# Performance work log

Measured on AMD Instinct MI355X. Metric: run time of the kernel, lower is better.

The kernel has to match this reference:

```python
import jax, jax.numpy as jnp
import numpy as np

K = 3  # kernel_size

def _extract_patches(x):
    # x: (b, n, h, w) -> (b, n, K*K, h, w), stride=1, padding=1 (zeros), row-major kernel order like nn.Unfold
    b, n, h, w = x.shape
    xp = jnp.pad(x, ((0, 0), (0, 0), (1, 1), (1, 1)))
    slices = [xp[:, :, i:i + h, j:j + w] for i in range(K) for j in range(K)]
    return jnp.stack(slices, axis=2)

def _conv3x3(x, w, b):
    # x: (b, cin, h, w), w: (cout, cin, 3, 3)
    y = jax.lax.conv_general_dilated(
        x, w, window_strides=(1, 1), padding=((1, 1), (1, 1)),
        dimension_numbers=('NCHW', 'OIHW', 'NCHW'))
    return y + b[None, :, None, None]

def setup_inputs() -> dict:
    key = jax.random.key(0)
    ks = jax.random.split(key, 6)
    b, n, h, w = 8, 256, 64, 64
    cout, r = 256, 4
    cm = n // r
    s = lambda fan: 1.0 / np.sqrt(fan)
    return {
        'x':    jax.random.normal(ks[0], (b, n, h, w), jnp.float32),
        'w_c1': jax.random.normal(ks[1], (cm, n), jnp.float32) * s(n),
        'b_c1': jnp.zeros((cm,), jnp.float32),
        'w_c2': jax.random.normal(ks[2], (n, cm), jnp.float32) * s(cm),
        'b_c2': jnp.zeros((n,), jnp.float32),
        'w_d1': jax.random.normal(ks[3], (cm, n, 3, 3), jnp.float32) * s(n * 9),
        'b_d1': jnp.zeros((cm,), jnp.float32),
        'w_d2': jax.random.normal(ks[4], (K * K, cm), jnp.float32) * s(cm),
        'b_d2': jnp.zeros((K * K,), jnp.float32),
        'W':    jax.random.normal(ks[5], (cout, n, K * K), jnp.float32) * s(n * K * K),
    }

def reference(x, w_c1, b_c1, w_c2, b_c2, w_d1, b_d1, w_d2, b_d2, W):
    # channel attention branch: 1x1 -> ReLU -> 1x1, output (b, n, h, w)
    yc = jax.nn.relu(jnp.einsum('bnhw,mn->bmhw', x, w_c1) + b_c1[None, :, None, None])
    c = jnp.einsum('bmhw,nm->bnhw', yc, w_c2) + b_c2[None, :, None, None]
    # kernel (spatial) attention branch: 3x3 -> ReLU -> 1x1, output (b, K*K, h, w)
    yd = jax.nn.relu(_conv3x3(x, w_d1, b_d1))
    d = jnp.einsum('bmhw,km->bkhw', yd, w_d2) + b_d2[None, :, None, None]
    # unfold and modulate: (b, n, K*K, h, w)
    patches = _extract_patches(x)
    attn = 1.0 + jnp.tanh(d[:, None, :, :, :] + c[:, :, None, :, :])
    # conv3d with (out, in, K*K, 1, 1) weight == per-pixel contraction over (n, K*K)
    out = jnp.einsum('bnkhw,onk->bohw', patches * attn, W)
    return out
```

## Files before the change

kernel.cpp:

```cpp
#include <hip/hip_runtime.h>
#include <hip/hip_bf16.h>
#include <stdint.h>

typedef __attribute__((ext_vector_type(8))) short bf16x8;
typedef __attribute__((ext_vector_type(4))) short bf16x4;
typedef __attribute__((ext_vector_type(4))) float f32x4;
typedef __attribute__((ext_vector_type(4))) int   i32x4;
typedef __attribute__((ext_vector_type(2))) int   i32x2;

#define DEV static __device__ __forceinline__

DEV float bf2f(short s) {
    unsigned u = ((unsigned)(unsigned short)s) << 16;
    return __builtin_bit_cast(float, u);
}
DEV short f2bf(float f) {
    unsigned u = __builtin_bit_cast(unsigned, f);
    unsigned r = u + 0x7fffu + ((u >> 16) & 1u);
    return (short)(r >> 16);
}
DEV unsigned cvt_pk_bf16(float lo, float hi) {
    unsigned r;
    asm("v_cvt_pk_bf16_f32 %0, %1, %2" : "=v"(r) : "v"(lo), "v"(hi));
    return r;
}

#define PTOT 32768
#define NEXP2 (-2.885390081777927f)

#define WS_WC1F 0
#define WS_WC2F 32768
#define WS_WD1F 65536
#define WS_WF   360448
#define WS_EKT  1540096
#define WS_EN   2719744
#define WS_XT   19496960

__global__ __launch_bounds__(256) void k_prep_all(const float* __restrict__ W, const float* __restrict__ w_d1,
                                              const float* __restrict__ w_c1, const float* __restrict__ w_c2,
                                              const float* __restrict__ x,
                                              short* __restrict__ Wf, short* __restrict__ wd1f,
                                              short* __restrict__ wc1f, short* __restrict__ wc2f,
                                              short* __restrict__ xT8) {
    __shared__ short t[64 * 74];
    const int tid = threadIdx.x;
    if (blockIdx.x < 3008) {
        int tt = blockIdx.x * 256 + tid;
        if (tt < 589824) {
            int i = tt & 7, lane = (tt >> 3) & 63, ot = (tt >> 9) & 15, kt = tt >> 13;
            int o = ot * 16 + (lane & 15);
            int n = (kt & 7) * 32 + (lane >> 4) * 8 + i;
            Wf[tt] = f2bf(2.0f * W[o * 2304 + n * 9 + (kt >> 3)]);
        } else if (tt < 589824 + 147456) {
            int t2 = tt - 589824;
            int i = t2 & 7, lane = (t2 >> 3) & 63, wv = (t2 >> 9) & 3, kc = t2 >> 11;
            int m = wv * 16 + (lane & 15);
            int n = (kc & 7) * 32 + (lane >> 4) * 8 + i;
            wd1f[t2] = f2bf(w_d1[m * 2304 + n * 9 + (kc >> 3)]);
        } else if (tt < 589824 + 147456 + 16384) {
            int t3 = tt - (589824 + 147456);
            int i = t3 & 7, lane = (t3 >> 3) & 63, wv = (t3 >> 9) & 3, s = t3 >> 11;
            int m = wv * 16 + (lane & 15);
            int n = s * 32 + (lane >> 4) * 8 + i;
            wc1f[t3] = f2bf(w_c1[m * 256 + n]);
        } else if (tt < 589824 + 147456 + 32768) {
            int t4 = tt - (589824 + 147456 + 16384);
            int i = t4 & 7, lane = (t4 >> 3) & 63, ot = (t4 >> 9) & 15, s = t4 >> 13;
            int o = ot * 16 + (lane & 15);
            int kk = s * 32 + (lane >> 4) * 8 + i;
            wc2f[t4] = f2bf(w_c2[o * 64 + kk]);
        }
        return;
    }
    const int bid = blockIdx.x - 3008;
    const int rw = ((bid & 7) << 6) + (bid >> 3);
    const int b = rw >> 6, hr = rw & 63;
    const int hp = hr + 1;
    #define XI(HP, NP, WP) ((((size_t)(b) * 66 + (HP)) * 32 + (NP)) * 66 + (WP)) * 8
    if (tid < 64) {
        int np = tid & 31, wp = (tid & 32) ? 65 : 0;
        *(i32x4*)(xT8 + XI(hp, np, wp)) = i32x4{0, 0, 0, 0};
    }
    if (hr == 0) {
        for (int i = tid; i < 2 * 32 * 66; i += 256) {
            int pl = (i >= 32 * 66) ? 65 : 0;
            int rem = (i >= 32 * 66) ? i - 32 * 66 : i;
            int np = rem / 66, wp = rem - np * 66;
            *(i32x4*)(xT8 + XI(pl, np, wp)) = i32x4{0, 0, 0, 0};
        }
    }
    const int dn = tid >> 6, w = tid & 63;
    for (int p = 0; p < 4; ++p) {
        __syncthreads();
        #pragma unroll
        for (int jj = 0; jj < 16; ++jj) {
            int n = p * 64 + dn * 16 + jj;
            t[w * 74 + dn * 16 + jj] = f2bf(x[(((size_t)(b * 256 + n) * 64) + hr) * 64 + w]);
        }
        __syncthreads();
        #pragma unroll
        for (int q = 0; q < 2; ++q) {
            int nl = q * 4 + dn;
            *(bf16x8*)(xT8 + XI(hp, p * 8 + nl, w + 1)) = *(const bf16x8*)(t + w * 74 + nl * 8);
        }
    }
    #undef XI
}

#define BR_YD_OFF  9216
#define BR_ENT_OFF (BR_YD_OFF + 17152)
#define BR_TOTAL   (BR_ENT_OFF + 33792)

__global__ __launch_bounds__(512, 4) void k_branch(const short* __restrict__ xT8,
        const float* __restrict__ b_c1, const float* __restrict__ b_c2,
        const float* __restrict__ b_d1, const float* __restrict__ w_d2, const float* __restrict__ b_d2,
        const short* __restrict__ wc1f, const short* __restrict__ wc2f, const short* __restrict__ wd1f,
        short* __restrict__ enF, float* __restrict__ ekT) {
    extern __shared__ char smem[];
    short* yc  = (short*)smem;
    float* ydl = (float*)(smem + BR_YD_OFF);
    short* ent = (short*)(smem + BR_ENT_OFF);

    const int rw = ((blockIdx.x & 7) << 6) + (blockIdx.x >> 3);
    const int b = rw >> 6, h = rw & 63;
    const int p0 = rw << 6;
    const int tid = threadIdx.x;
    const int lane = tid & 63, wave = tid >> 6;
    const int l16 = lane & 15, lg = lane >> 4;
    const int wn = wave & 3, wm = wave >> 2;
    const int cm = wn * 16 + l16;
    const size_t b66h = (size_t)(b * 66 + h);
    const int wcol = wm * 32 + l16;

    #define CONV_A(DST, KC) {                                                           \
        int k9_ = (KC) >> 3;                                                            \
        int kh_ = (k9_ * 11) >> 5, kw_ = k9_ - 3 * kh_;                                 \
        const short* xa_ = xT8 + (((b66h + kh_) * 32 + ((KC) & 7) * 4 + lg) * 66        \
                                  + wcol + kw_) * 8;                                    \
        DST[0] = *(const bf16x8*)(xa_);                                                 \
        DST[1] = *(const bf16x8*)(xa_ + 128);                                           \
    }

    {
        f32x4 acc[2] = {};
        const short* wp_ = wc1f + wn * 512 + lane * 8;
        const short* xg1 = xT8 + (((b66h + 1) * 32 + lg) * 66 + wcol + 1) * 8;
        bf16x8 bcur = *(const bf16x8*)(wp_);
        bf16x8 a0 = *(const bf16x8*)(xg1), a1 = *(const bf16x8*)(xg1 + 128);
        #pragma unroll
        for (int s = 0; s < 8; ++s) {
            bf16x8 bc = bcur, c0 = a0, c1 = a1;
            if (s < 7) {
                bcur = *(const bf16x8*)(wp_ + (s + 1) * 2048);
                a0 = *(const bf16x8*)(xg1 + (s + 1) * 2112);
                a1 = *(const bf16x8*)(xg1 + (s + 1) * 2112 + 128);
            }
            acc[0] = __builtin_amdgcn_mfma_f32_16x16x32_bf16(c0, bc, acc[0], 0, 0, 0);
            acc[1] = __builtin_amdgcn_mfma_f32_16x16x32_bf16(c1, bc, acc[1], 0, 0, 0);
        }
        float bias = b_c1[cm];
        #pragma unroll
        for (int mt = 0; mt < 2; ++mt)
            #pragma unroll
            for (int r = 0; r < 4; ++r) {
                int px = wm * 32 + mt * 16 + lg * 4 + r;
                float v = acc[mt][r] + bias;
                yc[px * 72 + cm] = f2bf(v > 0.f ? v : 0.f);
            }
    }

    {
        f32x4 acc[2] = {};
        const short* wp_ = wd1f + wn * 512 + lane * 8;
        bf16x8 b0 = *(const bf16x8*)(wp_);
        bf16x8 b1 = *(const bf16x8*)(wp_ + 2048);
        bf16x8 b2 = *(const bf16x8*)(wp_ + 4096);
        bf16x8 aA[2], aB[2], aC[2];
        CONV_A(aA, 0) CONV_A(aB, 1) CONV_A(aC, 2)
        for (int kc = 0; kc < 72; kc += 3) {
            {
                bf16x8 c0 = aA[0], c1 = aA[1], bc = b0;
                int cn = (kc + 3 < 72) ? kc + 3 : 71;
                CONV_A(aA, cn)
                b0 = *(const bf16x8*)(wp_ + cn * 2048);
                acc[0] = __builtin_amdgcn_mfma_f32_16x16x32_bf16(c0, bc, acc[0], 0, 0, 0);
                acc[1] = __builtin_amdgcn_mfma_f32_16x16x32_bf16(c1, bc, acc[1], 0, 0, 0);
            }
            {
                bf16x8 c0 = aB[0], c1 = aB[1], bc = b1;
                int cn = (kc + 4 < 72) ? kc + 4 : 71;
                CONV_A(aB, cn)
                b1 = *(const bf16x8*)(wp_ + cn * 2048);
                acc[0] = __builtin_amdgcn_mfma_f32_16x16x32_bf16(c0, bc, acc[0], 0, 0, 0);
                acc[1] = __builtin_amdgcn_mfma_f32_16x16x32_bf16(c1, bc, acc[1], 0, 0, 0);
            }
            {
                bf16x8 c0 = aC[0], c1 = aC[1], bc = b2;
                int cn = (kc + 5 < 72) ? kc + 5 : 71;
                CONV_A(aC, cn)
                b2 = *(const bf16x8*)(wp_ + cn * 2048);
                acc[0] = __builtin_amdgcn_mfma_f32_16x16x32_bf16(c0, bc, acc[0], 0, 0, 0);
                acc[1] = __builtin_amdgcn_mfma_f32_16x16x32_bf16(c1, bc, acc[1], 0, 0, 0);
            }
        }
        float bias = b_d1[cm];
        #pragma unroll
        for (int mt = 0; mt < 2; ++mt)
            #pragma unroll
            for (int r = 0; r < 4; ++r) {
                int px = wm * 32 + mt * 16 + lg * 4 + r;
                float v = acc[mt][r] + bias;
                ydl[px * 67 + cm] = v > 0.f ? v : 0.f;
            }
    }
    #undef CONV_A
    __syncthreads();

    {
        f32x4 acc[2][4] = {};
        #pragma unroll
        for (int s = 0; s < 2; ++s) {
            int k0 = s * 32;
            bf16x8 afr[2], bfr[4];
            #pragma unroll
            for (int mt = 0; mt < 2; ++mt)
                afr[mt] = *(const bf16x8*)(yc + (wm * 32 + mt * 16 + l16) * 72 + k0 + lg * 8);
            #pragma unroll
            for (int nt = 0; nt < 4; ++nt)
                bfr[nt] = *(const bf16x8*)(wc2f + s * 8192 + (wn * 4 + nt) * 512 + lane * 8);
            #pragma unroll
            for (int mt = 0; mt < 2; ++mt)
                #pragma unroll
                for (int nt = 0; nt < 4; ++nt)
                    acc[mt][nt] = __builtin_amdgcn_mfma_f32_16x16x32_bf16(afr[mt], bfr[nt], acc[mt][nt], 0, 0, 0);
        }
        #pragma unroll
        for (int nt = 0; nt < 4; ++nt) {
            int nc = wn * 64 + nt * 16 + l16;
            float bias = b_c2[nc];
            #pragma unroll
            for (int mt = 0; mt < 2; ++mt)
                #pragma unroll
                for (int r = 0; r < 4; ++r) {
                    int px = wm * 32 + mt * 16 + lg * 4 + r;
                    float cv = acc[mt][nt][r] + bias;
                    ent[px * 264 + nc] = f2bf(exp2f(NEXP2 * cv));
                }
        }
    }

    for (int t = tid; t < 576; t += 512) {
        int k = t >> 6, px = t & 63;
        float sum = b_d2[k];
        const float* yr = ydl + px * 67;
        const float* wr = w_d2 + k * 64;
        #pragma unroll 8
        for (int m = 0; m < 64; ++m) sum += yr[m] * wr[m];
        ekT[(size_t)k * PTOT + p0 + px] = exp2f(NEXP2 * sum);
    }
    __syncthreads();

    for (int i = tid; i < 2048; i += 512) {
        int px = i & 63, seg = i >> 6;
        *(bf16x8*)(enF + (size_t)p0 * 256 + (seg >> 2) * 2048 + (seg & 3) * 512 + px * 8)
            = *(const bf16x8*)(ent + px * 264 + seg * 8);
    }
}

#define FN6_EKL   16384
#define FN6_TOTAL 18688

__global__ __launch_bounds__(512, 4) void k_final(const short* __restrict__ xT8,
        const short* __restrict__ Wf, const short* __restrict__ enF, const float* __restrict__ ekT,
        float* __restrict__ out) {
    extern __shared__ char smem[];
    short* zq0 = (short*)smem;
    short* zq1 = (short*)(smem + 4096);
    short* zq2 = (short*)(smem + 8192);
    short* zq3 = (short*)(smem + 12288);
    float* ekl = (float*)(smem + FN6_EKL);

    const int rw = ((blockIdx.x & 7) << 6) + (blockIdx.x >> 3);
    const int b = rw >> 6, h = rw & 63;
    const int p0 = rw << 6;
    const int tid = threadIdx.x;
    const int lane = tid & 63, wave = tid >> 6;
    const int l16 = lane & 15, lg = lane >> 4;

    for (int i = tid; i < 576; i += 512)
        ekl[i] = ekT[(size_t)(i >> 6) * PTOT + p0 + (i & 63)];

    const size_t b66h = (size_t)(b * 66 + h);
    const int zpx = lane;
    const int wh = wave >> 1, wl = wave & 1;
    const short* xb0 = xT8 + (b66h * 32 + wh) * 528 + zpx * 8 + wl * 4;
    bf16x4 e_regs[8];
    {
        const short* enb = enF + (size_t)p0 * 256 + wh * 512 + zpx * 8 + wl * 4;
        #pragma unroll
        for (int c8 = 0; c8 < 8; ++c8) e_regs[c8] = *(const bf16x4*)(enb + c8 * 2048);
    }
    const int zwoff = (zpx >> 4) * 512 + ((zpx & 15) + wh * 16) * 8 + wl * 4;
    const short* wb0 = Wf + (wave * 2 + 0) * 512 + lane * 8;
    const short* wb1 = Wf + (wave * 2 + 1) * 512 + lane * 8;

    #define ZQ(I) ((I) == 0 ? zq0 : (I) == 1 ? zq1 : (I) == 2 ? zq2 : zq3)

    bf16x4 xrA, xrB;
    #define XLOADA(KC2) {                                                               \
        int k3_ = (KC2) >> 3, c8_ = (KC2) & 7;                                          \
        int kh_ = (k3_ * 11) >> 5, kw_ = k3_ - 3 * kh_;                                 \
        xrA = *(const bf16x4*)(xb0 + kh_ * 16896 + c8_ * 2112 + kw_ * 8);               \
    }
    #define XLOADB(KC2) {                                                               \
        int k3_ = (KC2) >> 3, c8_ = (KC2) & 7;                                          \
        int kh_ = (k3_ * 11) >> 5, kw_ = k3_ - 3 * kh_;                                 \
        xrB = *(const bf16x4*)(xb0 + kh_ * 16896 + c8_ * 2112 + kw_ * 8);               \
    }
    #define ZBUILDX(ZBUF, EKROW, EIDX, XR) {                                            \
        bf16x4 er = e_regs[EIDX];                                                       \
        float ekv = ekl[(EKROW) * 64 + zpx];                                            \
        float q0 = __builtin_fmaf(ekv, bf2f(er[0]), 1.0f);                              \
        float q1 = __builtin_fmaf(ekv, bf2f(er[1]), 1.0f);                              \
        float q2 = __builtin_fmaf(ekv, bf2f(er[2]), 1.0f);                              \
        float q3 = __builtin_fmaf(ekv, bf2f(er[3]), 1.0f);                              \
        i32x2 zz;                                                                       \
        zz[0] = cvt_pk_bf16(bf2f(XR[0]) * __builtin_amdgcn_rcpf(q0),                    \
                            bf2f(XR[1]) * __builtin_amdgcn_rcpf(q1));                   \
        zz[1] = cvt_pk_bf16(bf2f(XR[2]) * __builtin_amdgcn_rcpf(q2),                    \
                            bf2f(XR[3]) * __builtin_amdgcn_rcpf(q3));                   \
        *(i32x2*)((ZBUF) + zwoff) = zz;                                                 \
    }

    bf16x8 Be[2], Bo[2];
    Be[0] = *(const bf16x8*)(wb0);          Be[1] = *(const bf16x8*)(wb1);
    Bo[0] = *(const bf16x8*)(wb0 + 8192);   Bo[1] = *(const bf16x8*)(wb1 + 8192);
    XLOADA(0) XLOADB(1)
    __syncthreads();
    ZBUILDX(zq0, 0, 0, xrA)
    ZBUILDX(zq1, 0, 1, xrB)
    XLOADA(2) XLOADB(3)
    __syncthreads();

    f32x4 acc[4][2] = {};

    #define PHASE(C8, P1, P2, EKR) {                                                    \
        short* zE = ZQ((C8) & 3);                                                       \
        short* zO = ZQ(((C8) + 1) & 3);                                                 \
        bf16x8 afr[4];                                                                  \
        _Pragma("unroll")                                                               \
        for (int mt = 0; mt < 4; ++mt)                                                  \
            afr[mt] = *(const bf16x8*)(zE + mt * 512 + lane * 8);                       \
        __builtin_amdgcn_s_setprio(1);                                                  \
        _Pragma("unroll")                                                               \
        for (int mt = 0; mt < 4; ++mt) {                                                \
            acc[mt][0] = __builtin_amdgcn_mfma_f32_16x16x32_bf16(afr[mt], Be[0], acc[mt][0], 0, 0, 0); \
            acc[mt][1] = __builtin_amdgcn_mfma_f32_16x16x32_bf16(afr[mt], Be[1], acc[mt][1], 0, 0, 0); \
        }                                                                               \
        __builtin_amdgcn_s_setprio(0);                                                  \
        if (P1) {                                                                       \
            int kb2_ = (k3 * 8 + (C8) + 2) * 8192;                                      \
            Be[0] = *(const bf16x8*)(wb0 + kb2_);                                       \
            Be[1] = *(const bf16x8*)(wb1 + kb2_);                                       \
            ZBUILDX(ZQ(((C8) + 2) & 3), EKR, ((C8) + 2) & 7, xrA)                       \
        }                                                                               \
        if (P2) XLOADA(k3 * 8 + (C8) + 4)                                               \
        _Pragma("unroll")                                                               \
        for (int mt = 0; mt < 4; ++mt)                                                  \
            afr[mt] = *(const bf16x8*)(zO + mt * 512 + lane * 8);                       \
        __builtin_amdgcn_s_setprio(1);                                                  \
        _Pragma("unroll")                                                               \
        for (int mt = 0; mt < 4; ++mt) {                                                \
            acc[mt][0] = __builtin_amdgcn_mfma_f32_16x16x32_bf16(afr[mt], Bo[0], acc[mt][0], 0, 0, 0); \
            acc[mt][1] = __builtin_amdgcn_mfma_f32_16x16x32_bf16(afr[mt], Bo[1], acc[mt][1], 0, 0, 0); \
        }                                                                               \
        __builtin_amdgcn_s_setprio(0);                                                  \
        if (P1) {                                                                       \
            int kb3_ = (k3 * 8 + (C8) + 3) * 8192;                                      \
            Bo[0] = *(const bf16x8*)(wb0 + kb3_);                                       \
            Bo[1] = *(const bf16x8*)(wb1 + kb3_);                                       \
            ZBUILDX(ZQ(((C8) + 3) & 3), EKR, ((C8) + 3) & 7, xrB)                       \
        }                                                                               \
        if (P2) XLOADB(k3 * 8 + (C8) + 5)                                               \
        __syncthreads();                                                                \
    }

    for (int k3 = 0; k3 < 8; ++k3) {
        PHASE(0, 1, 1, k3) PHASE(2, 1, 1, k3)
        PHASE(4, 1, 1, k3) PHASE(6, 1, 1, k3 + 1)
    }
    {
        const int k3 = 8;
        PHASE(0, 1, 1, k3) PHASE(2, 1, 1, k3)
        PHASE(4, 1, 0, k3) PHASE(6, 0, 0, k3)
    }
    #undef PHASE
    #undef ZBUILDX
    #undef XLOADA
    #undef XLOADB
    #undef ZQ

    #pragma unroll
    for (int mt = 0; mt < 4; ++mt)
        #pragma unroll
        for (int nt = 0; nt < 2; ++nt) {
            int o = wave * 32 + nt * 16 + l16;
            float* d = out + (((size_t)b * 256 + o) * 64 + h) * 64 + mt * 16 + lg * 4;
            *(f32x4*)d = acc[mt][nt];
        }
}

extern "C" void kernel_launch(void* const* d_in, const int* in_sizes, int n_in,
                              void* d_out, int out_size, void* d_ws, size_t ws_size,
                              hipStream_t stream) {
    const float* x    = (const float*)d_in[0];
    const float* w_c1 = (const float*)d_in[1];
    const float* b_c1 = (const float*)d_in[2];
    const float* w_c2 = (const float*)d_in[3];
    const float* b_c2 = (const float*)d_in[4];
    const float* w_d1 = (const float*)d_in[5];
    const float* b_d1 = (const float*)d_in[6];
    const float* w_d2 = (const float*)d_in[7];
    const float* b_d2 = (const float*)d_in[8];
    const float* Wt   = (const float*)d_in[9];
    float* out = (float*)d_out;
    char* ws = (char*)d_ws;

    short* wc1f = (short*)(ws + WS_WC1F);
    short* wc2f = (short*)(ws + WS_WC2F);
    short* wd1f = (short*)(ws + WS_WD1F);
    short* Wf   = (short*)(ws + WS_WF);
    float* ekT  = (float*)(ws + WS_EKT);
    short* enF  = (short*)(ws + WS_EN);
    short* xT8  = (short*)(ws + WS_XT);

    (void)hipFuncSetAttribute((const void*)k_branch, hipFuncAttributeMaxDynamicSharedMemorySize, BR_TOTAL);
    (void)hipFuncSetAttribute((const void*)k_final,  hipFuncAttributeMaxDynamicSharedMemorySize, FN6_TOTAL);

    k_prep_all<<<3520, 256, 0, stream>>>(Wt, w_d1, w_c1, w_c2, x, Wf, wd1f, wc1f, wc2f, xT8);
    k_branch<<<512, 512, BR_TOTAL, stream>>>(xT8, b_c1, b_c2, b_d1, w_d2, b_d2, wc1f, wc2f, wd1f, enF, ekT);
    k_final<<<512, 512, FN6_TOTAL, stream>>>(xT8, Wf, enF, ekT, out);
}
```

Before: 103.8 us.

## Fuse branch and final kernels, keeping attention terms in shared memory

Merges the attention-branch kernel and the final modulation/contraction kernel into one launch per row. The per-pixel channel and kernel attention exponentials now stay in LDS and go straight into the final stage, so they are no longer written to and reread from global workspace. This removes a kernel launch and a global round trip of about 16 MB of bf16 plus the fp32 kernel-attention terms. In exchange, LDS use per block rises to about 62 KB, which may lower occupancy, and ZQ buffers are aliased over the yc/yd region, which relies on the barrier ordering being correct.

After: 93.14 us. -10.3%, faster.

```diff
diff --git a/kernel.cpp b/kernel.cpp
--- a/kernel.cpp
+++ b/kernel.cpp
@@ -32,8 +32,6 @@
 #define WS_WC2F 32768
 #define WS_WD1F 65536
 #define WS_WF   360448
-#define WS_EKT  1540096
-#define WS_EN   2719744
 #define WS_XT   19496960
 
 __global__ __launch_bounds__(256) void k_prep_all(const float* __restrict__ W, const float* __restrict__ w_d1,
@@ -107,23 +105,26 @@
     #undef XI
 }
 
-#define BR_YD_OFF  9216
-#define BR_ENT_OFF (BR_YD_OFF + 17152)
-#define BR_TOTAL   (BR_ENT_OFF + 33792)
-
-__global__ __launch_bounds__(512, 4) void k_branch(const short* __restrict__ xT8,
+#define FZ_YC    33792
+#define FZ_YD    43008
+#define FZ_ZQ    33792
+#define FZ_EKL   60160
+#define FZ_TOTAL 62464
+
+__global__ __launch_bounds__(512, 4) void k_fused(const short* __restrict__ xT8,
         const float* __restrict__ b_c1, const float* __restrict__ b_c2,
         const float* __restrict__ b_d1, const float* __restrict__ w_d2, const float* __restrict__ b_d2,
         const short* __restrict__ wc1f, const short* __restrict__ wc2f, const short* __restrict__ wd1f,
-        short* __restrict__ enF, float* __restrict__ ekT) {
+        const short* __restrict__ Wf, float* __restrict__ out) {
     extern __shared__ char smem[];
-    short* yc  = (short*)smem;
-    float* ydl = (float*)(smem + BR_YD_OFF);
-    short* ent = (short*)(smem + BR_ENT_OFF);
+    short* ent = (short*)smem;
+    short* yc  = (short*)(smem + FZ_YC);
+    float* ydl = (float*)(smem + FZ_YD);
+    short* zqb = (short*)(smem + FZ_ZQ);
+    float* ekl = (float*)(smem + FZ_EKL);
 
     const int rw = ((blockIdx.x & 7) << 6) + (blockIdx.x >> 3);
     const int b = rw >> 6, h = rw & 63;
-    const int p0 = rw << 6;
     const int tid = threadIdx.x;
     const int lane = tid & 63, wave = tid >> 6;
     const int l16 = lane & 15, lg = lane >> 4;
@@ -256,55 +257,24 @@
         const float* wr = w_d2 + k * 64;
         #pragma unroll 8
         for (int m = 0; m < 64; ++m) sum += yr[m] * wr[m];
-        ekT[(size_t)k * PTOT + p0 + px] = exp2f(NEXP2 * sum);
+        ekl[t] = exp2f(NEXP2 * sum);
     }
     __syncthreads();
 
-    for (int i = tid; i < 2048; i += 512) {
-        int px = i & 63, seg = i >> 6;
-        *(bf16x8*)(enF + (size_t)p0 * 256 + (seg >> 2) * 2048 + (seg & 3) * 512 + px * 8)
-            = *(const bf16x8*)(ent + px * 264 + seg * 8);
-    }
-}
-
-#define FN6_EKL   16384
-#define FN6_TOTAL 18688
-
-__global__ __launch_bounds__(512, 4) void k_final(const short* __restrict__ xT8,
-        const short* __restrict__ Wf, const short* __restrict__ enF, const float* __restrict__ ekT,
-        float* __restrict__ out) {
-    extern __shared__ char smem[];
-    short* zq0 = (short*)smem;
-    short* zq1 = (short*)(smem + 4096);
-    short* zq2 = (short*)(smem + 8192);
-    short* zq3 = (short*)(smem + 12288);
-    float* ekl = (float*)(smem + FN6_EKL);
-
-    const int rw = ((blockIdx.x & 7) << 6) + (blockIdx.x >> 3);
-    const int b = rw >> 6, h = rw & 63;
-    const int p0 = rw << 6;
-    const int tid = threadIdx.x;
-    const int lane = tid & 63, wave = tid >> 6;
-    const int l16 = lane & 15, lg = lane >> 4;
-
-    for (int i = tid; i < 576; i += 512)
-        ekl[i] = ekT[(size_t)(i >> 6) * PTOT + p0 + (i & 63)];
-
-    const size_t b66h = (size_t)(b * 66 + h);
     const int zpx = lane;
     const int wh = wave >> 1, wl = wave & 1;
     const short* xb0 = xT8 + (b66h * 32 + wh) * 528 + zpx * 8 + wl * 4;
     bf16x4 e_regs[8];
     {
-        const short* enb = enF + (size_t)p0 * 256 + wh * 512 + zpx * 8 + wl * 4;
-        #pragma unroll
-        for (int c8 = 0; c8 < 8; ++c8) e_regs[c8] = *(const bf16x4*)(enb + c8 * 2048);
+        const short* entp = ent + lane * 264 + wh * 8 + wl * 4;
+        #pragma unroll
+        for (int c8 = 0; c8 < 8; ++c8) e_regs[c8] = *(const bf16x4*)(entp + c8 * 32);
     }
     const int zwoff = (zpx >> 4) * 512 + ((zpx & 15) + wh * 16) * 8 + wl * 4;
     const short* wb0 = Wf + (wave * 2 + 0) * 512 + lane * 8;
     const short* wb1 = Wf + (wave * 2 + 1) * 512 + lane * 8;
 
-    #define ZQ(I) ((I) == 0 ? zq0 : (I) == 1 ? zq1 : (I) == 2 ? zq2 : zq3)
+    #define ZQ(I) (zqb + (I) * 2048)
 
     bf16x4 xrA, xrB;
     #define XLOADA(KC2) {                                                               \
@@ -336,9 +306,8 @@
     Be[0] = *(const bf16x8*)(wb0);          Be[1] = *(const bf16x8*)(wb1);
     Bo[0] = *(const bf16x8*)(wb0 + 8192);   Bo[1] = *(const bf16x8*)(wb1 + 8192);
     XLOADA(0) XLOADB(1)
-    __syncthreads();
-    ZBUILDX(zq0, 0, 0, xrA)
-    ZBUILDX(zq1, 0, 1, xrB)
+    ZBUILDX(ZQ(0), 0, 0, xrA)
+    ZBUILDX(ZQ(1), 0, 1, xrB)
     XLOADA(2) XLOADB(3)
     __syncthreads();
 
@@ -430,14 +399,11 @@
     short* wc2f = (short*)(ws + WS_WC2F);
     short* wd1f = (short*)(ws + WS_WD1F);
     short* Wf   = (short*)(ws + WS_WF);
-    float* ekT  = (float*)(ws + WS_EKT);
-    short* enF  = (short*)(ws + WS_EN);
     short* xT8  = (short*)(ws + WS_XT);
 
-    (void)hipFuncSetAttribute((const void*)k_branch, hipFuncAttributeMaxDynamicSharedMemorySize, BR_TOTAL);
-    (void)hipFuncSetAttribute((const void*)k_final,  hipFuncAttributeMaxDynamicSharedMemorySize, FN6_TOTAL);
+    (void)hipFuncSetAttribute((const void*)k_fused, hipFuncAttributeMaxDynamicSharedMemorySize, FZ_TOTAL);
 
     k_prep_all<<<3520, 256, 0, stream>>>(Wt, w_d1, w_c1, w_c2, x, Wf, wd1f, wc1f, wc2f, xT8);
-    k_branch<<<512, 512, BR_TOTAL, stream>>>(xT8, b_c1, b_c2, b_d1, w_d2, b_d2, wc1f, wc2f, wd1f, enF, ekT);
-    k_final<<<512, 512, FN6_TOTAL, stream>>>(xT8, Wf, enF, ekT, out);
-}
+    k_fused<<<512, 512, FZ_TOTAL, stream>>>(xT8, b_c1, b_c2, b_d1, w_d2, b_d2,
+                                            wc1f, wc2f, wd1f, Wf, out);
+}
```
